# Performance work log

Measured on AMD Instinct MI355X. Metric: run time of the kernel, lower is better.

## Reference

```python
import jax, jax.numpy as jnp
import numpy as np

B, T, V, F = 32, 128, 128, 64
K_ORDER = 3
N_FILT = 64

def setup_inputs() -> dict:
    key = jax.random.key(0)
    k1, k2, k3 = jax.random.split(key, 3)
    x = jax.random.normal(k1, (B, T, V, F), dtype=jnp.float32)
    W = jax.random.uniform(k2, (B, V, V), dtype=jnp.float32)  # learned adjacency, nonneg
    # keras 'uniform' initializer default range [-0.05, 0.05]
    Theta = jax.random.uniform(k3, (K_ORDER, F, N_FILT), dtype=jnp.float32, minval=-0.05, maxval=0.05)
    return {"x": x, "W": W, "Theta": Theta}

def reference(x, W, Theta):
    # x: (B,T,V,F), W: (B,V,V), Theta: (k,F,O)
    k = Theta.shape[0]
    v = x.shape[2]
    eye = jnp.eye(v, dtype=x.dtype)
    deg = jnp.sum(W, axis=1)                      # (B,V) -- sum over axis=1 as in K.sum(W, axis=1)
    D = eye[None, :, :] * deg[:, :, None]         # matrix_diag(deg)
    L = D - W
    L_t = L - eye[None, :, :]                     # 2*L/lambda_max - I with lambda_max=2
    chebs = [jnp.broadcast_to(eye[None, :, :], W.shape), L_t]
    for i in range(2, k):
        # NOTE: elementwise multiply, faithful to the original tf code (tf `*`)
        chebs.append(2.0 * L_t * chebs[-1] - chebs[-2])
    Tk = jnp.stack(chebs, axis=0)                 # (k,B,V,V)
    # out[b,t,u,o] = sum_{k,v,f} Tk[k,b,v,u] * x[b,t,v,f] * Theta[k,f,o]
    # (T_k transposed matmul graph_signal, then dot with theta_k, summed over k and t-batched)
    out = jnp.einsum('kbvu,btvf,kfo->btuo', Tk, x, Theta)
    return jax.nn.relu(out)
```

## Files before the change

### kernel.cpp

```cpp
#include <hip/hip_runtime.h>

typedef __attribute__((ext_vector_type(8))) short bf16x8;
typedef __attribute__((ext_vector_type(4))) float f32x4;

namespace {

constexpr int B = 32, T = 128, V = 128, F = 64, O = 64;

constexpr size_t WS_THT_OFF = (size_t)B * 64 * 64 * 8 * 2;
constexpr size_t WS_LDG_OFF = WS_THT_OFF + 1536 * 8 * 2;

__device__ inline unsigned short f2bf(float f) {
    unsigned u = __builtin_bit_cast(unsigned, f);
    u += 0x7FFFu + ((u >> 16) & 1u);
    return (unsigned short)(u >> 16);
}

__global__ __launch_bounds__(256) void prep(const float* __restrict__ W,
                                            const float* __restrict__ Theta,
                                            unsigned short* __restrict__ acat_f,
                                            unsigned short* __restrict__ tht_f,
                                            float* __restrict__ ldg) {
    const int tid = threadIdx.x;
    if (blockIdx.x == B) {
        for (int i = 0; i < 6; ++i) {
            int fi = tid + i * 256;
            int ks = fi / 768, rem = fi % 768;
            int nf = rem >> 6, lane = rem & 63;
            int n = nf * 16 + (lane & 15);
            int f0 = ks * 32 + (lane >> 4) * 8;
            unsigned short vals[8];
#pragma unroll
            for (int j = 0; j < 8; ++j) {
                int f = f0 + j;
                float v;
                if (n < 64)       v = Theta[f * 64 + n] - Theta[2 * 4096 + f * 64 + n];
                else if (n < 128) v = Theta[4096 + f * 64 + (n - 64)];
                else              v = Theta[2 * 4096 + f * 64 + (n - 128)];
                vals[j] = f2bf(v);
            }
            *(bf16x8*)(tht_f + (size_t)fi * 8) = *(bf16x8*)vals;
        }
        return;
    }
    const int b = blockIdx.x;
    const float* Wb = W + (size_t)b * V * V;
    __shared__ float Wl[V][V + 1];
    for (int i = 0; i < V * V / 256; ++i) {
        int idx = tid + i * 256;
        Wl[idx >> 7][idx & 127] = Wb[idx];
    }
    __syncthreads();
    if (tid < V) {
        float s = 0.f;
        for (int i = 0; i < V; ++i) s += Wl[i][tid];
        ldg[b * V + tid] = s - 1.0f - Wl[tid][tid];
    }
    unsigned short* ab_f = acat_f + (size_t)b * 32768;
    for (int i = 0; i < 16; ++i) {
        int fi = tid + i * 256;
        int ks = fi >> 9, rem = fi & 511;
        int r2 = rem >> 6, lane = rem & 63;
        int u = r2 * 16 + (lane & 15);
        int kv0 = ks * 32 + (lane >> 4) * 8;
        unsigned short vals[8];
#pragma unroll
        for (int j = 0; j < 8; ++j) {
            int kv = kv0 + j, v = kv & 127;
            float wv = Wl[v][u];
            float val = (v == u) ? 0.f : ((kv < 128) ? -wv : 2.f * wv * wv);
            vals[j] = f2bf(val);
        }
        *(bf16x8*)(ab_f + (size_t)fi * 8) = *(bf16x8*)vals;
    }
}

__global__ __launch_bounds__(256, 4) void graph_conv_main(
    const float* __restrict__ x, const unsigned short* __restrict__ acat_f,
    const unsigned short* __restrict__ tht_f, const float* __restrict__ ldg,
    float* __restrict__ out) {
    const int t = blockIdx.x, b = blockIdx.y;
    const int tid = threadIdx.x;
    const int lane = tid & 63, w = tid >> 6;
    const int lr = lane & 15, lg = lane >> 4;

    __shared__ __align__(16) unsigned short xsz[8192];
    __shared__ __align__(16) unsigned short zc1[8192];

    const float* xbt = x + ((size_t)(b * T + t)) * (V * F);
    const float4* xslab = (const float4*)(xbt + w * 32 * 64);
    char* xbase = (char*)xsz + w * 4096;
#pragma unroll
    for (int i = 0; i < 8; ++i) {
        float4 q = xslab[i * 64 + lane];
        int f4 = i * 64 + lane;
        int row = f4 >> 4, c4 = f4 & 15;
        uint2 p;
        p.x = f2bf(q.x) | ((unsigned)f2bf(q.y) << 16);
        p.y = f2bf(q.z) | ((unsigned)f2bf(q.w) << 16);
        *(uint2*)(xbase + row * 128 + ((c4 * 8) ^ ((row & 7) << 4))) = p;
    }

    bf16x8 xa[2][2];
#pragma unroll
    for (int vf = 0; vf < 2; ++vf) {
        int row = 16 * vf + lr;
#pragma unroll
        for (int ks = 0; ks < 2; ++ks)
            xa[vf][ks] = *(const bf16x8*)(xbase + row * 128 + ((ks * 64 + lg * 16) ^ ((row & 7) << 4)));
    }

    f32x4 acc[2][4], z[2][4];
#pragma unroll
    for (int vf = 0; vf < 2; ++vf)
#pragma unroll
        for (int of = 0; of < 4; ++of) {
            acc[vf][of] = (f32x4){0.f, 0.f, 0.f, 0.f};
            z[vf][of] = (f32x4){0.f, 0.f, 0.f, 0.f};
        }

#pragma unroll
    for (int ks = 0; ks < 2; ++ks)
#pragma unroll
        for (int nf = 0; nf < 8; ++nf) {
            bf16x8 tb = *(const bf16x8*)(tht_f + ((size_t)(ks * 12 + nf) * 64 + lane) * 8);
            if (nf < 4) {
                acc[0][nf] = __builtin_amdgcn_mfma_f32_16x16x32_bf16(xa[0][ks], tb, acc[0][nf], 0, 0, 0);
                acc[1][nf] = __builtin_amdgcn_mfma_f32_16x16x32_bf16(xa[1][ks], tb, acc[1][nf], 0, 0, 0);
            } else {
                z[0][nf - 4] = __builtin_amdgcn_mfma_f32_16x16x32_bf16(xa[0][ks], tb, z[0][nf - 4], 0, 0, 0);
                z[1][nf - 4] = __builtin_amdgcn_mfma_f32_16x16x32_bf16(xa[1][ks], tb, z[1][nf - 4], 0, 0, 0);
            }
        }

    const float* ldb = ldg + b * V;
    f32x4 ldv[2];
#pragma unroll
    for (int vf = 0; vf < 2; ++vf) {
        ldv[vf] = *(const f32x4*)(ldb + w * 32 + 16 * vf + lg * 4);
#pragma unroll
        for (int of = 0; of < 4; ++of) acc[vf][of] += ldv[vf] * z[vf][of];
    }
#pragma unroll
    for (int vf = 0; vf < 2; ++vf) {
        int vcol = w * 32 + 16 * vf + lg * 4;
#pragma unroll
        for (int of = 0; of < 4; ++of) {
            int rowz = of * 16 + lr;
            f32x4 zv = z[vf][of];
            uint2 q;
            q.x = f2bf(zv[0]) | ((unsigned)f2bf(zv[1]) << 16);
            q.y = f2bf(zv[2]) | ((unsigned)f2bf(zv[3]) << 16);
            *(uint2*)((char*)zc1 + rowz * 256 + ((vcol * 2) ^ ((rowz & 7) << 4))) = q;
            z[vf][of] = (f32x4){0.f, 0.f, 0.f, 0.f};
        }
    }

#pragma unroll
    for (int ks = 0; ks < 2; ++ks)
#pragma unroll
        for (int nf = 0; nf < 4; ++nf) {
            bf16x8 tb = *(const bf16x8*)(tht_f + ((size_t)(ks * 12 + 8 + nf) * 64 + lane) * 8);
            z[0][nf] = __builtin_amdgcn_mfma_f32_16x16x32_bf16(xa[0][ks], tb, z[0][nf], 0, 0, 0);
            z[1][nf] = __builtin_amdgcn_mfma_f32_16x16x32_bf16(xa[1][ks], tb, z[1][nf], 0, 0, 0);
        }

#pragma unroll
    for (int vf = 0; vf < 2; ++vf) {
        f32x4 ld2 = 2.0f * ldv[vf] * ldv[vf];
#pragma unroll
        for (int of = 0; of < 4; ++of) acc[vf][of] += ld2 * z[vf][of];
    }

    __syncthreads();

#pragma unroll
    for (int vf = 0; vf < 2; ++vf) {
        int vcol = w * 32 + 16 * vf + lg * 4;
#pragma unroll
        for (int of = 0; of < 4; ++of) {
            int rowz = of * 16 + lr;
            f32x4 zv = z[vf][of];
            uint2 q;
            q.x = f2bf(zv[0]) | ((unsigned)f2bf(zv[1]) << 16);
            q.y = f2bf(zv[2]) | ((unsigned)f2bf(zv[3]) << 16);
            *(uint2*)((char*)xsz + rowz * 256 + ((vcol * 2) ^ ((rowz & 7) << 4))) = q;
        }
    }
    __syncthreads();

#pragma unroll
    for (int ks = 0; ks < 8; ++ks) {
        bf16x8 af[2];
#pragma unroll
        for (int uf = 0; uf < 2; ++uf)
            af[uf] = *(const bf16x8*)(acat_f +
                     (((size_t)b * 64 + ks * 8 + (w * 2 + uf)) * 64 + lane) * 8);
        const char* zsrc = (ks < 4) ? (const char*)zc1 : (const char*)xsz;
        const int kcol = (ks & 3) * 64 + lg * 16;
#pragma unroll
        for (int of = 0; of < 4; ++of) {
            int rowz = of * 16 + lr;
            bf16x8 zb = *(const bf16x8*)(zsrc + rowz * 256 + (kcol ^ ((rowz & 7) << 4)));
            acc[0][of] = __builtin_amdgcn_mfma_f32_16x16x32_bf16(af[0], zb, acc[0][of], 0, 0, 0);
            acc[1][of] = __builtin_amdgcn_mfma_f32_16x16x32_bf16(af[1], zb, acc[1][of], 0, 0, 0);
        }
    }

    float* obt = out + ((size_t)(b * T + t)) * (V * O);
#pragma unroll
    for (int vf = 0; vf < 2; ++vf)
#pragma unroll
        for (int of = 0; of < 4; ++of)
#pragma unroll
            for (int j = 0; j < 4; ++j) {
                int u = w * 32 + 16 * vf + lg * 4 + j;
                int o = of * 16 + lr;
                float r = acc[vf][of][j];
                obt[u * 64 + o] = r > 0.f ? r : 0.f;
            }
}

}

extern "C" void kernel_launch(void* const* d_in, const int* in_sizes, int n_in,
                              void* d_out, int out_size, void* d_ws, size_t ws_size,
                              hipStream_t stream) {
    const float* x = (const float*)d_in[0];
    const float* W = (const float*)d_in[1];
    const float* Theta = (const float*)d_in[2];
    float* outp = (float*)d_out;

    unsigned short* acat_f = (unsigned short*)d_ws;
    unsigned short* tht_f = (unsigned short*)((char*)d_ws + WS_THT_OFF);
    float* ldg = (float*)((char*)d_ws + WS_LDG_OFF);

    prep<<<B + 1, 256, 0, stream>>>(W, Theta, acat_f, tht_f, ldg);
    graph_conv_main<<<dim3(T, B), 256, 0, stream>>>(x, acat_f, tht_f, ldg, outp);
}
```

Baseline: 92.87 us.

## Process multiple timesteps per block with double-buffered async x loads to LDS

Each block now handles TPB=8 timesteps in a loop. The x slab for the next timestep is prefetched with global_load_lds into a second fp32 LDS buffer while the current one is computed. The fp32-to-bf16 conversion moves to the LDS reads. This is meant to hide global load latency and amortize per-block setup, at the cost of much more LDS (64KB of fp32 buffers plus the z buffers), lower occupancy (launch bounds 2) and a grid of only 512 blocks.

```diff
diff --git a/kernel.cpp b/kernel.cpp
--- a/kernel.cpp
+++ b/kernel.cpp
@@ -6,6 +6,7 @@
 namespace {
 
 constexpr int B = 32, T = 128, V = 128, F = 64, O = 64;
+constexpr int TPB = 8;
 
 constexpr size_t WS_THT_OFF = (size_t)B * 64 * 64 * 8 * 2;
 constexpr size_t WS_LDG_OFF = WS_THT_OFF + 1536 * 8 * 2;
@@ -14,6 +15,15 @@
     unsigned u = __builtin_bit_cast(unsigned, f);
     u += 0x7FFFu + ((u >> 16) & 1u);
     return (unsigned short)(u >> 16);
+}
+
+__device__ inline bf16x8 pack8(const float4 a, const float4 b) {
+    uint4 u;
+    u.x = f2bf(a.x) | ((unsigned)f2bf(a.y) << 16);
+    u.y = f2bf(a.z) | ((unsigned)f2bf(a.w) << 16);
+    u.z = f2bf(b.x) | ((unsigned)f2bf(b.y) << 16);
+    u.w = f2bf(b.z) | ((unsigned)f2bf(b.w) << 16);
+    return __builtin_bit_cast(bf16x8, u);
 }
 
 __global__ __launch_bounds__(256) void prep(const float* __restrict__ W,
@@ -75,150 +85,169 @@
     }
 }
 
-__global__ __launch_bounds__(256, 4) void graph_conv_main(
+__global__ __launch_bounds__(256, 2) void graph_conv_main(
     const float* __restrict__ x, const unsigned short* __restrict__ acat_f,
     const unsigned short* __restrict__ tht_f, const float* __restrict__ ldg,
     float* __restrict__ out) {
-    const int t = blockIdx.x, b = blockIdx.y;
+    const int t0 = blockIdx.x * TPB, b = blockIdx.y;
     const int tid = threadIdx.x;
     const int lane = tid & 63, w = tid >> 6;
     const int lr = lane & 15, lg = lane >> 4;
 
-    __shared__ __align__(16) unsigned short xsz[8192];
-    __shared__ __align__(16) unsigned short zc1[8192];
-
-    const float* xbt = x + ((size_t)(b * T + t)) * (V * F);
-    const float4* xslab = (const float4*)(xbt + w * 32 * 64);
-    char* xbase = (char*)xsz + w * 4096;
-#pragma unroll
-    for (int i = 0; i < 8; ++i) {
-        float4 q = xslab[i * 64 + lane];
-        int f4 = i * 64 + lane;
-        int row = f4 >> 4, c4 = f4 & 15;
-        uint2 p;
-        p.x = f2bf(q.x) | ((unsigned)f2bf(q.y) << 16);
-        p.y = f2bf(q.z) | ((unsigned)f2bf(q.w) << 16);
-        *(uint2*)(xbase + row * 128 + ((c4 * 8) ^ ((row & 7) << 4))) = p;
-    }
-
-    bf16x8 xa[2][2];
-#pragma unroll
-    for (int vf = 0; vf < 2; ++vf) {
-        int row = 16 * vf + lr;
+    __shared__ __align__(16) float xbuf[2][V * F];
+    __shared__ __align__(16) unsigned short zc1[4096];
+    __shared__ __align__(16) unsigned short zc2[4096];
+
+    const float* xb = x + ((size_t)(b * T + t0)) * (V * F);
+    const float* ldb = ldg + b * V;
+
+    auto stage = [&](int tt, int buf) {
+        const float* src = xb + (size_t)tt * (V * F);
+        char* lbase = (char*)&xbuf[buf][0] + w * 8192;
+#pragma unroll
+        for (int j = 0; j < 8; ++j) {
+            int n = w * 512 + j * 64 + lane;
+            int row = n >> 4;
+            int c = (n & 15) ^ (row & 7);
+            const float* g = src + row * 64 + c * 4;
+            __builtin_amdgcn_global_load_lds(
+                (const __attribute__((address_space(1))) void*)g,
+                (__attribute__((address_space(3))) void*)(lbase + j * 1024), 16, 0, 0);
+        }
+    };
+
+    stage(0, 0);
+    __syncthreads();
+    int cur = 0;
+
+    for (int tt = 0; tt < TPB; ++tt) {
+        if (tt + 1 < TPB) stage(tt + 1, cur ^ 1);
+
+        const char* xc = (const char*)&xbuf[cur][0];
+        bf16x8 xa[2][2];
+#pragma unroll
+        for (int vf = 0; vf < 2; ++vf) {
+            const int row = w * 32 + vf * 16 + lr;
+            const int rb = row * 256, rs = row & 7;
+#pragma unroll
+            for (int ks = 0; ks < 2; ++ks) {
+                const int c0 = ks * 8 + lg * 2;
+                float4 a = *(const float4*)(xc + rb + ((c0 ^ rs) << 4));
+                float4 bq = *(const float4*)(xc + rb + (((c0 + 1) ^ rs) << 4));
+                xa[vf][ks] = pack8(a, bq);
+            }
+        }
+
+        f32x4 acc[2][4], z[2][4];
+#pragma unroll
+        for (int vf = 0; vf < 2; ++vf)
+#pragma unroll
+            for (int of = 0; of < 4; ++of) {
+                acc[vf][of] = (f32x4){0.f, 0.f, 0.f, 0.f};
+                z[vf][of] = (f32x4){0.f, 0.f, 0.f, 0.f};
+            }
+
 #pragma unroll
         for (int ks = 0; ks < 2; ++ks)
-            xa[vf][ks] = *(const bf16x8*)(xbase + row * 128 + ((ks * 64 + lg * 16) ^ ((row & 7) << 4)));
-    }
-
-    f32x4 acc[2][4], z[2][4];
-#pragma unroll
-    for (int vf = 0; vf < 2; ++vf)
-#pragma unroll
-        for (int of = 0; of < 4; ++of) {
-            acc[vf][of] = (f32x4){0.f, 0.f, 0.f, 0.f};
-            z[vf][of] = (f32x4){0.f, 0.f, 0.f, 0.f};
-        }
-
-#pragma unroll
-    for (int ks = 0; ks < 2; ++ks)
-#pragma unroll
-        for (int nf = 0; nf < 8; ++nf) {
-            bf16x8 tb = *(const bf16x8*)(tht_f + ((size_t)(ks * 12 + nf) * 64 + lane) * 8);
-            if (nf < 4) {
-                acc[0][nf] = __builtin_amdgcn_mfma_f32_16x16x32_bf16(xa[0][ks], tb, acc[0][nf], 0, 0, 0);
-                acc[1][nf] = __builtin_amdgcn_mfma_f32_16x16x32_bf16(xa[1][ks], tb, acc[1][nf], 0, 0, 0);
-            } else {
-                z[0][nf - 4] = __builtin_amdgcn_mfma_f32_16x16x32_bf16(xa[0][ks], tb, z[0][nf - 4], 0, 0, 0);
-                z[1][nf - 4] = __builtin_amdgcn_mfma_f32_16x16x32_bf16(xa[1][ks], tb, z[1][nf - 4], 0, 0, 0);
-            }
-        }
-
-    const float* ldb = ldg + b * V;
-    f32x4 ldv[2];
-#pragma unroll
-    for (int vf = 0; vf < 2; ++vf) {
-        ldv[vf] = *(const f32x4*)(ldb + w * 32 + 16 * vf + lg * 4);
-#pragma unroll
-        for (int of = 0; of < 4; ++of) acc[vf][of] += ldv[vf] * z[vf][of];
-    }
-#pragma unroll
-    for (int vf = 0; vf < 2; ++vf) {
-        int vcol = w * 32 + 16 * vf + lg * 4;
-#pragma unroll
-        for (int of = 0; of < 4; ++of) {
-            int rowz = of * 16 + lr;
-            f32x4 zv = z[vf][of];
-            uint2 q;
-            q.x = f2bf(zv[0]) | ((unsigned)f2bf(zv[1]) << 16);
-            q.y = f2bf(zv[2]) | ((unsigned)f2bf(zv[3]) << 16);
-            *(uint2*)((char*)zc1 + rowz * 256 + ((vcol * 2) ^ ((rowz & 7) << 4))) = q;
-            z[vf][of] = (f32x4){0.f, 0.f, 0.f, 0.f};
-        }
-    }
-
-#pragma unroll
-    for (int ks = 0; ks < 2; ++ks)
-#pragma unroll
-        for (int nf = 0; nf < 4; ++nf) {
-            bf16x8 tb = *(const bf16x8*)(tht_f + ((size_t)(ks * 12 + 8 + nf) * 64 + lane) * 8);
-            z[0][nf] = __builtin_amdgcn_mfma_f32_16x16x32_bf16(xa[0][ks], tb, z[0][nf], 0, 0, 0);
-            z[1][nf] = __builtin_amdgcn_mfma_f32_16x16x32_bf16(xa[1][ks], tb, z[1][nf], 0, 0, 0);
-        }
-
-#pragma unroll
-    for (int vf = 0; vf < 2; ++vf) {
-        f32x4 ld2 = 2.0f * ldv[vf] * ldv[vf];
-#pragma unroll
-        for (int of = 0; of < 4; ++of) acc[vf][of] += ld2 * z[vf][of];
-    }
-
-    __syncthreads();
-
-#pragma unroll
-    for (int vf = 0; vf < 2; ++vf) {
-        int vcol = w * 32 + 16 * vf + lg * 4;
-#pragma unroll
-        for (int of = 0; of < 4; ++of) {
-            int rowz = of * 16 + lr;
-            f32x4 zv = z[vf][of];
-            uint2 q;
-            q.x = f2bf(zv[0]) | ((unsigned)f2bf(zv[1]) << 16);
-            q.y = f2bf(zv[2]) | ((unsigned)f2bf(zv[3]) << 16);
-            *(uint2*)((char*)xsz + rowz * 256 + ((vcol * 2) ^ ((rowz & 7) << 4))) = q;
-        }
-    }
-    __syncthreads();
-
-#pragma unroll
-    for (int ks = 0; ks < 8; ++ks) {
-        bf16x8 af[2];
-#pragma unroll
-        for (int uf = 0; uf < 2; ++uf)
-            af[uf] = *(const bf16x8*)(acat_f +
-                     (((size_t)b * 64 + ks * 8 + (w * 2 + uf)) * 64 + lane) * 8);
-        const char* zsrc = (ks < 4) ? (const char*)zc1 : (const char*)xsz;
-        const int kcol = (ks & 3) * 64 + lg * 16;
-#pragma unroll
-        for (int of = 0; of < 4; ++of) {
-            int rowz = of * 16 + lr;
-            bf16x8 zb = *(const bf16x8*)(zsrc + rowz * 256 + (kcol ^ ((rowz & 7) << 4)));
-            acc[0][of] = __builtin_amdgcn_mfma_f32_16x16x32_bf16(af[0], zb, acc[0][of], 0, 0, 0);
-            acc[1][of] = __builtin_amdgcn_mfma_f32_16x16x32_bf16(af[1], zb, acc[1][of], 0, 0, 0);
-        }
-    }
-
-    float* obt = out + ((size_t)(b * T + t)) * (V * O);
-#pragma unroll
-    for (int vf = 0; vf < 2; ++vf)
-#pragma unroll
-        for (int of = 0; of < 4; ++of)
-#pragma unroll
-            for (int j = 0; j < 4; ++j) {
-                int u = w * 32 + 16 * vf + lg * 4 + j;
-                int o = of * 16 + lr;
-                float r = acc[vf][of][j];
-                obt[u * 64 + o] = r > 0.f ? r : 0.f;
-            }
+#pragma unroll
+            for (int nf = 0; nf < 8; ++nf) {
+                bf16x8 tb = *(const bf16x8*)(tht_f + ((size_t)(ks * 12 + nf) * 64 + lane) * 8);
+                if (nf < 4) {
+                    acc[0][nf] = __builtin_amdgcn_mfma_f32_16x16x32_bf16(xa[0][ks], tb, acc[0][nf], 0, 0, 0);
+                    acc[1][nf] = __builtin_amdgcn_mfma_f32_16x16x32_bf16(xa[1][ks], tb, acc[1][nf], 0, 0, 0);
+                } else {
+                    z[0][nf - 4] = __builtin_amdgcn_mfma_f32_16x16x32_bf16(xa[0][ks], tb, z[0][nf - 4], 0, 0, 0);
+                    z[1][nf - 4] = __builtin_amdgcn_mfma_f32_16x16x32_bf16(xa[1][ks], tb, z[1][nf - 4], 0, 0, 0);
+                }
+            }
+
+        f32x4 ldv[2];
+#pragma unroll
+        for (int vf = 0; vf < 2; ++vf) {
+            ldv[vf] = *(const f32x4*)(ldb + w * 32 + 16 * vf + lg * 4);
+#pragma unroll
+            for (int of = 0; of < 4; ++of) acc[vf][of] += ldv[vf] * z[vf][of];
+        }
+#pragma unroll
+        for (int vf = 0; vf < 2; ++vf) {
+            const int vcol = w * 32 + 16 * vf + lg * 4;
+#pragma unroll
+            for (int of = 0; of < 4; ++of) {
+                const int rowz = of * 16 + lr;
+                f32x4 zv = z[vf][of];
+                uint2 q;
+                q.x = f2bf(zv[0]) | ((unsigned)f2bf(zv[1]) << 16);
+                q.y = f2bf(zv[2]) | ((unsigned)f2bf(zv[3]) << 16);
+                *(uint2*)((char*)zc1 + rowz * 256 + ((vcol * 2) ^ ((rowz & 7) << 4))) = q;
+                z[vf][of] = (f32x4){0.f, 0.f, 0.f, 0.f};
+            }
+        }
+
+#pragma unroll
+        for (int ks = 0; ks < 2; ++ks)
+#pragma unroll
+            for (int nf = 0; nf < 4; ++nf) {
+                bf16x8 tb = *(const bf16x8*)(tht_f + ((size_t)(ks * 12 + 8 + nf) * 64 + lane) * 8);
+                z[0][nf] = __builtin_amdgcn_mfma_f32_16x16x32_bf16(xa[0][ks], tb, z[0][nf], 0, 0, 0);
+                z[1][nf] = __builtin_amdgcn_mfma_f32_16x16x32_bf16(xa[1][ks], tb, z[1][nf], 0, 0, 0);
+            }
+
+#pragma unroll
+        for (int vf = 0; vf < 2; ++vf) {
+            f32x4 ld2 = 2.0f * ldv[vf] * ldv[vf];
+#pragma unroll
+            for (int of = 0; of < 4; ++of) acc[vf][of] += ld2 * z[vf][of];
+        }
+#pragma unroll
+        for (int vf = 0; vf < 2; ++vf) {
+            const int vcol = w * 32 + 16 * vf + lg * 4;
+#pragma unroll
+            for (int of = 0; of < 4; ++of) {
+                const int rowz = of * 16 + lr;
+                f32x4 zv = z[vf][of];
+                uint2 q;
+                q.x = f2bf(zv[0]) | ((unsigned)f2bf(zv[1]) << 16);
+                q.y = f2bf(zv[2]) | ((unsigned)f2bf(zv[3]) << 16);
+                *(uint2*)((char*)zc2 + rowz * 256 + ((vcol * 2) ^ ((rowz & 7) << 4))) = q;
+            }
+        }
+
+        __syncthreads();
+
+#pragma unroll
+        for (int ks = 0; ks < 8; ++ks) {
+            bf16x8 af[2];
+#pragma unroll
+            for (int uf = 0; uf < 2; ++uf)
+                af[uf] = *(const bf16x8*)(acat_f +
+                         (((size_t)b * 64 + ks * 8 + (w * 2 + uf)) * 64 + lane) * 8);
+            const char* zsrc = (ks < 4) ? (const char*)zc1 : (const char*)zc2;
+            const int kcol = (ks & 3) * 64 + lg * 16;
+#pragma unroll
+            for (int of = 0; of < 4; ++of) {
+                const int rowz = of * 16 + lr;
+                bf16x8 zb = *(const bf16x8*)(zsrc + rowz * 256 + (kcol ^ ((rowz & 7) << 4)));
+                acc[0][of] = __builtin_amdgcn_mfma_f32_16x16x32_bf16(af[0], zb, acc[0][of], 0, 0, 0);
+                acc[1][of] = __builtin_amdgcn_mfma_f32_16x16x32_bf16(af[1], zb, acc[1][of], 0, 0, 0);
+            }
+        }
+
+        float* obt = out + ((size_t)(b * T + t0 + tt)) * (V * O);
+#pragma unroll
+        for (int vf = 0; vf < 2; ++vf)
+#pragma unroll
+            for (int of = 0; of < 4; ++of)
+#pragma unroll
+                for (int j = 0; j < 4; ++j) {
+                    const int u = w * 32 + 16 * vf + lg * 4 + j;
+                    const int o = of * 16 + lr;
+                    const float r = acc[vf][of][j];
+                    obt[u * 64 + o] = r > 0.f ? r : 0.f;
+                }
+
+        __syncthreads();
+        cur ^= 1;
+    }
 }
 
 }
@@ -236,5 +265,5 @@
     float* ldg = (float*)((char*)d_ws + WS_LDG_OFF);
 
     prep<<<B + 1, 256, 0, stream>>>(W, Theta, acat_f, tht_f, ldg);
-    graph_conv_main<<<dim3(T, B), 256, 0, stream>>>(x, acat_f, tht_f, ldg, outp);
-}
+    graph_conv_main<<<dim3(T / TPB, B), 256, 0, stream>>>(x, acat_f, tht_f, ldg, outp);
+}
```

Measured after the change: 177.5 us. 91.2% more time.

## Process 16 timesteps per block with double-buffered x prefetch and register-resident A

Applied to the files above, without the earlier changes.

Each 512-thread block now handles 16 timesteps of one batch, two at a time, with the next pair of x slices prefetched into registers and stored to a double-buffered LDS area. Theta fragments are loaded once into LDS via global_load_lds, and the graph operator fragments are held in registers across iterations. This amortizes the per-block loads of acat and theta and overlaps x loading with compute. In exchange it greatly reduces the number of blocks, relies on a large LDS footprint, and adds register pressure.

```diff
diff --git a/kernel.cpp b/kernel.cpp
--- a/kernel.cpp
+++ b/kernel.cpp
@@ -6,6 +6,7 @@
 namespace {
 
 constexpr int B = 32, T = 128, V = 128, F = 64, O = 64;
+constexpr int TPB = 16;
 
 constexpr size_t WS_THT_OFF = (size_t)B * 64 * 64 * 8 * 2;
 constexpr size_t WS_LDG_OFF = WS_THT_OFF + 1536 * 8 * 2;
@@ -75,150 +76,188 @@
     }
 }
 
-__global__ __launch_bounds__(256, 4) void graph_conv_main(
+__global__ __launch_bounds__(512, 2) void graph_conv_main(
     const float* __restrict__ x, const unsigned short* __restrict__ acat_f,
     const unsigned short* __restrict__ tht_f, const float* __restrict__ ldg,
     float* __restrict__ out) {
-    const int t = blockIdx.x, b = blockIdx.y;
+    const int t0 = blockIdx.x * TPB, b = blockIdx.y;
     const int tid = threadIdx.x;
     const int lane = tid & 63, w = tid >> 6;
+    const int q = w & 3;
+    const int p = w >> 2;
     const int lr = lane & 15, lg = lane >> 4;
 
-    __shared__ __align__(16) unsigned short xsz[8192];
-    __shared__ __align__(16) unsigned short zc1[8192];
-
-    const float* xbt = x + ((size_t)(b * T + t)) * (V * F);
-    const float4* xslab = (const float4*)(xbt + w * 32 * 64);
-    char* xbase = (char*)xsz + w * 4096;
-#pragma unroll
-    for (int i = 0; i < 8; ++i) {
-        float4 q = xslab[i * 64 + lane];
-        int f4 = i * 64 + lane;
-        int row = f4 >> 4, c4 = f4 & 15;
-        uint2 p;
-        p.x = f2bf(q.x) | ((unsigned)f2bf(q.y) << 16);
-        p.y = f2bf(q.z) | ((unsigned)f2bf(q.w) << 16);
-        *(uint2*)(xbase + row * 128 + ((c4 * 8) ^ ((row & 7) << 4))) = p;
-    }
-
-    bf16x8 xa[2][2];
+    __shared__ __align__(16) unsigned short tht_s[12288];
+    __shared__ __align__(16) unsigned short xbuf[2][2][8192];
+    __shared__ __align__(16) unsigned short zc1[2][8192];
+    __shared__ __align__(16) unsigned short zc2[2][8192];
+
+    const float* xb = x + ((size_t)(b * T + t0)) * (V * F);
+
+#pragma unroll
+    for (int i = 0; i < 3; ++i) {
+        int c = tid + i * 512;
+        __builtin_amdgcn_global_load_lds(
+            (const __attribute__((address_space(1))) void*)(tht_f + c * 8),
+            (__attribute__((address_space(3))) void*)(tht_s + c * 8), 16, 0, 0);
+    }
+
+    bf16x8 af_r[2][8];
+#pragma unroll
+    for (int ks = 0; ks < 8; ++ks)
+#pragma unroll
+        for (int uf = 0; uf < 2; ++uf)
+            af_r[uf][ks] = *(const bf16x8*)(acat_f +
+                (((size_t)b * 64 + ks * 8 + 2 * q + uf) * 64 + lane) * 8);
+
+    const float* ldb = ldg + b * V;
+    f32x4 ldv[2], ld2v[2];
 #pragma unroll
     for (int vf = 0; vf < 2; ++vf) {
-        int row = 16 * vf + lr;
+        ldv[vf] = *(const f32x4*)(ldb + 32 * q + 16 * vf + lg * 4);
+        ld2v[vf] = 2.0f * ldv[vf] * ldv[vf];
+    }
+
+    float4 pf[8];
+    auto load_pf = [&](int pr) {
+        const float4* s0 = (const float4*)(xb + (size_t)(2 * pr) * (V * F));
+        const float4* s1 = (const float4*)(xb + (size_t)(2 * pr + 1) * (V * F));
+#pragma unroll
+        for (int i = 0; i < 4; ++i) pf[i] = s0[tid + i * 512];
+#pragma unroll
+        for (int i = 0; i < 4; ++i) pf[4 + i] = s1[tid + i * 512];
+    };
+    auto store_pf = [&](int buf) {
+#pragma unroll
+        for (int i = 0; i < 8; ++i) {
+            int pp = i >> 2;
+            int f4 = tid + (i & 3) * 512;
+            int row = f4 >> 4, c4 = f4 & 15;
+            uint2 qq;
+            qq.x = f2bf(pf[i].x) | ((unsigned)f2bf(pf[i].y) << 16);
+            qq.y = f2bf(pf[i].z) | ((unsigned)f2bf(pf[i].w) << 16);
+            *(uint2*)((char*)xbuf + (size_t)(buf * 2 + pp) * 16384 +
+                      row * 128 + ((c4 * 8) ^ ((row & 7) << 4))) = qq;
+        }
+    };
+
+    load_pf(0);
+    store_pf(0);
+    __syncthreads();
+    int cur = 0;
+
+    for (int it = 0; it < TPB / 2; ++it) {
+        if (it + 1 < TPB / 2) load_pf(it + 1);
+
+        const char* xc = (const char*)xbuf + (size_t)(cur * 2 + p) * 16384;
+        bf16x8 xa[2][2];
+#pragma unroll
+        for (int vf = 0; vf < 2; ++vf) {
+            const int row = 32 * q + 16 * vf + lr;
+            const int rb = row * 128, rs = (row & 7) << 4;
+#pragma unroll
+            for (int ks = 0; ks < 2; ++ks)
+                xa[vf][ks] = *(const bf16x8*)(xc + rb + ((ks * 64 + lg * 16) ^ rs));
+        }
+
+        f32x4 acc[2][4], z[2][4];
+#pragma unroll
+        for (int vf = 0; vf < 2; ++vf)
+#pragma unroll
+            for (int of = 0; of < 4; ++of) {
+                acc[vf][of] = (f32x4){0.f, 0.f, 0.f, 0.f};
+                z[vf][of] = (f32x4){0.f, 0.f, 0.f, 0.f};
+            }
+
 #pragma unroll
         for (int ks = 0; ks < 2; ++ks)
-            xa[vf][ks] = *(const bf16x8*)(xbase + row * 128 + ((ks * 64 + lg * 16) ^ ((row & 7) << 4)));
-    }
-
-    f32x4 acc[2][4], z[2][4];
-#pragma unroll
-    for (int vf = 0; vf < 2; ++vf)
-#pragma unroll
-        for (int of = 0; of < 4; ++of) {
-            acc[vf][of] = (f32x4){0.f, 0.f, 0.f, 0.f};
-            z[vf][of] = (f32x4){0.f, 0.f, 0.f, 0.f};
-        }
-
-#pragma unroll
-    for (int ks = 0; ks < 2; ++ks)
-#pragma unroll
-        for (int nf = 0; nf < 8; ++nf) {
-            bf16x8 tb = *(const bf16x8*)(tht_f + ((size_t)(ks * 12 + nf) * 64 + lane) * 8);
-            if (nf < 4) {
-                acc[0][nf] = __builtin_amdgcn_mfma_f32_16x16x32_bf16(xa[0][ks], tb, acc[0][nf], 0, 0, 0);
-                acc[1][nf] = __builtin_amdgcn_mfma_f32_16x16x32_bf16(xa[1][ks], tb, acc[1][nf], 0, 0, 0);
-            } else {
-                z[0][nf - 4] = __builtin_amdgcn_mfma_f32_16x16x32_bf16(xa[0][ks], tb, z[0][nf - 4], 0, 0, 0);
-                z[1][nf - 4] = __builtin_amdgcn_mfma_f32_16x16x32_bf16(xa[1][ks], tb, z[1][nf - 4], 0, 0, 0);
-            }
-        }
-
-    const float* ldb = ldg + b * V;
-    f32x4 ldv[2];
-#pragma unroll
-    for (int vf = 0; vf < 2; ++vf) {
-        ldv[vf] = *(const f32x4*)(ldb + w * 32 + 16 * vf + lg * 4);
-#pragma unroll
-        for (int of = 0; of < 4; ++of) acc[vf][of] += ldv[vf] * z[vf][of];
-    }
-#pragma unroll
-    for (int vf = 0; vf < 2; ++vf) {
-        int vcol = w * 32 + 16 * vf + lg * 4;
-#pragma unroll
-        for (int of = 0; of < 4; ++of) {
-            int rowz = of * 16 + lr;
-            f32x4 zv = z[vf][of];
-            uint2 q;
-            q.x = f2bf(zv[0]) | ((unsigned)f2bf(zv[1]) << 16);
-            q.y = f2bf(zv[2]) | ((unsigned)f2bf(zv[3]) << 16);
-            *(uint2*)((char*)zc1 + rowz * 256 + ((vcol * 2) ^ ((rowz & 7) << 4))) = q;
-            z[vf][of] = (f32x4){0.f, 0.f, 0.f, 0.f};
-        }
-    }
-
-#pragma unroll
-    for (int ks = 0; ks < 2; ++ks)
-#pragma unroll
-        for (int nf = 0; nf < 4; ++nf) {
-            bf16x8 tb = *(const bf16x8*)(tht_f + ((size_t)(ks * 12 + 8 + nf) * 64 + lane) * 8);
-            z[0][nf] = __builtin_amdgcn_mfma_f32_16x16x32_bf16(xa[0][ks], tb, z[0][nf], 0, 0, 0);
-            z[1][nf] = __builtin_amdgcn_mfma_f32_16x16x32_bf16(xa[1][ks], tb, z[1][nf], 0, 0, 0);
-        }
-
-#pragma unroll
-    for (int vf = 0; vf < 2; ++vf) {
-        f32x4 ld2 = 2.0f * ldv[vf] * ldv[vf];
-#pragma unroll
-        for (int of = 0; of < 4; ++of) acc[vf][of] += ld2 * z[vf][of];
-    }
-
-    __syncthreads();
-
-#pragma unroll
-    for (int vf = 0; vf < 2; ++vf) {
-        int vcol = w * 32 + 16 * vf + lg * 4;
-#pragma unroll
-        for (int of = 0; of < 4; ++of) {
-            int rowz = of * 16 + lr;
-            f32x4 zv = z[vf][of];
-            uint2 q;
-            q.x = f2bf(zv[0]) | ((unsigned)f2bf(zv[1]) << 16);
-            q.y = f2bf(zv[2]) | ((unsigned)f2bf(zv[3]) << 16);
-            *(uint2*)((char*)xsz + rowz * 256 + ((vcol * 2) ^ ((rowz & 7) << 4))) = q;
-        }
-    }
-    __syncthreads();
-
-#pragma unroll
-    for (int ks = 0; ks < 8; ++ks) {
-        bf16x8 af[2];
-#pragma unroll
-        for (int uf = 0; uf < 2; ++uf)
-            af[uf] = *(const bf16x8*)(acat_f +
-                     (((size_t)b * 64 + ks * 8 + (w * 2 + uf)) * 64 + lane) * 8);
-        const char* zsrc = (ks < 4) ? (const char*)zc1 : (const char*)xsz;
-        const int kcol = (ks & 3) * 64 + lg * 16;
-#pragma unroll
-        for (int of = 0; of < 4; ++of) {
-            int rowz = of * 16 + lr;
-            bf16x8 zb = *(const bf16x8*)(zsrc + rowz * 256 + (kcol ^ ((rowz & 7) << 4)));
-            acc[0][of] = __builtin_amdgcn_mfma_f32_16x16x32_bf16(af[0], zb, acc[0][of], 0, 0, 0);
-            acc[1][of] = __builtin_amdgcn_mfma_f32_16x16x32_bf16(af[1], zb, acc[1][of], 0, 0, 0);
-        }
-    }
-
-    float* obt = out + ((size_t)(b * T + t)) * (V * O);
-#pragma unroll
-    for (int vf = 0; vf < 2; ++vf)
-#pragma unroll
-        for (int of = 0; of < 4; ++of)
-#pragma unroll
-            for (int j = 0; j < 4; ++j) {
-                int u = w * 32 + 16 * vf + lg * 4 + j;
-                int o = of * 16 + lr;
-                float r = acc[vf][of][j];
-                obt[u * 64 + o] = r > 0.f ? r : 0.f;
-            }
+#pragma unroll
+            for (int nf = 0; nf < 8; ++nf) {
+                bf16x8 tb = *(const bf16x8*)(tht_s + ((ks * 12 + nf) * 64 + lane) * 8);
+                if (nf < 4) {
+                    acc[0][nf] = __builtin_amdgcn_mfma_f32_16x16x32_bf16(xa[0][ks], tb, acc[0][nf], 0, 0, 0);
+                    acc[1][nf] = __builtin_amdgcn_mfma_f32_16x16x32_bf16(xa[1][ks], tb, acc[1][nf], 0, 0, 0);
+                } else {
+                    z[0][nf - 4] = __builtin_amdgcn_mfma_f32_16x16x32_bf16(xa[0][ks], tb, z[0][nf - 4], 0, 0, 0);
+                    z[1][nf - 4] = __builtin_amdgcn_mfma_f32_16x16x32_bf16(xa[1][ks], tb, z[1][nf - 4], 0, 0, 0);
+                }
+            }
+
+        char* z1p = (char*)zc1 + (size_t)p * 16384;
+        char* z2p = (char*)zc2 + (size_t)p * 16384;
+#pragma unroll
+        for (int vf = 0; vf < 2; ++vf) {
+            const int vcol = 32 * q + 16 * vf + lg * 4;
+#pragma unroll
+            for (int of = 0; of < 4; ++of) {
+                acc[vf][of] += ldv[vf] * z[vf][of];
+                const int rowz = of * 16 + lr;
+                f32x4 zv = z[vf][of];
+                uint2 qq;
+                qq.x = f2bf(zv[0]) | ((unsigned)f2bf(zv[1]) << 16);
+                qq.y = f2bf(zv[2]) | ((unsigned)f2bf(zv[3]) << 16);
+                *(uint2*)(z1p + rowz * 256 + ((vcol * 2) ^ ((rowz & 7) << 4))) = qq;
+                z[vf][of] = (f32x4){0.f, 0.f, 0.f, 0.f};
+            }
+        }
+
+#pragma unroll
+        for (int ks = 0; ks < 2; ++ks)
+#pragma unroll
+            for (int nf = 0; nf < 4; ++nf) {
+                bf16x8 tb = *(const bf16x8*)(tht_s + ((ks * 12 + 8 + nf) * 64 + lane) * 8);
+                z[0][nf] = __builtin_amdgcn_mfma_f32_16x16x32_bf16(xa[0][ks], tb, z[0][nf], 0, 0, 0);
+                z[1][nf] = __builtin_amdgcn_mfma_f32_16x16x32_bf16(xa[1][ks], tb, z[1][nf], 0, 0, 0);
+            }
+
+#pragma unroll
+        for (int vf = 0; vf < 2; ++vf) {
+            const int vcol = 32 * q + 16 * vf + lg * 4;
+#pragma unroll
+            for (int of = 0; of < 4; ++of) {
+                acc[vf][of] += ld2v[vf] * z[vf][of];
+                const int rowz = of * 16 + lr;
+                f32x4 zv = z[vf][of];
+                uint2 qq;
+                qq.x = f2bf(zv[0]) | ((unsigned)f2bf(zv[1]) << 16);
+                qq.y = f2bf(zv[2]) | ((unsigned)f2bf(zv[3]) << 16);
+                *(uint2*)(z2p + rowz * 256 + ((vcol * 2) ^ ((rowz & 7) << 4))) = qq;
+            }
+        }
+
+        __syncthreads();
+
+#pragma unroll
+        for (int ks = 0; ks < 8; ++ks) {
+            const char* zsrc = (ks < 4) ? (const char*)z1p : (const char*)z2p;
+            const int kcol = (ks & 3) * 64 + lg * 16;
+#pragma unroll
+            for (int of = 0; of < 4; ++of) {
+                const int rowz = of * 16 + lr;
+                bf16x8 zb = *(const bf16x8*)(zsrc + rowz * 256 + (kcol ^ ((rowz & 7) << 4)));
+                acc[0][of] = __builtin_amdgcn_mfma_f32_16x16x32_bf16(af_r[0][ks], zb, acc[0][of], 0, 0, 0);
+                acc[1][of] = __builtin_amdgcn_mfma_f32_16x16x32_bf16(af_r[1][ks], zb, acc[1][of], 0, 0, 0);
+            }
+        }
+
+        if (it + 1 < TPB / 2) store_pf(cur ^ 1);
+
+        float* obt = out + ((size_t)(b * T + t0 + 2 * it + p)) * (V * O);
+#pragma unroll
+        for (int vf = 0; vf < 2; ++vf)
+#pragma unroll
+            for (int of = 0; of < 4; ++of)
+#pragma unroll
+                for (int j = 0; j < 4; ++j) {
+                    const int u = 32 * q + 16 * vf + lg * 4 + j;
+                    const int o = of * 16 + lr;
+                    const float r = acc[vf][of][j];
+                    obt[u * 64 + o] = r > 0.f ? r : 0.f;
+                }
+
+        __syncthreads();
+        cur ^= 1;
+    }
 }
 
 }
@@ -236,5 +275,5 @@
     float* ldg = (float*)((char*)d_ws + WS_LDG_OFF);
 
     prep<<<B + 1, 256, 0, stream>>>(W, Theta, acat_f, tht_f, ldg);
-    graph_conv_main<<<dim3(T, B), 256, 0, stream>>>(x, acat_f, tht_f, ldg, outp);
-}
+    graph_conv_main<<<dim3(T / TPB, B), 512, 0, stream>>>(x, acat_f, tht_f, ldg, outp);
+}
```

Measured after the change: 127.6 us. 37.4% more time.
